# Optimization experiments

Hardware: AMD Instinct MI355X
Metric: run time of the kernel (lower is better)

The kernel has to match this reference:

```python
import jax, jax.numpy as jnp
import numpy as np


def conv1x1(x, w, b):
    # x: [B,C,H,W], w: [O,C], b: [O] -> [B,O,H,W]
    return jnp.einsum('bchw,oc->bohw', x, w) + b[None, :, None, None]


def setup_inputs() -> dict:
    key = jax.random.key(0)
    ks = jax.random.split(key, 8)
    B, C, H, W = 16, 256, 64, 64
    Cq = C // 8
    x = jax.random.normal(ks[0], (B, C, H, W), dtype=jnp.float32)
    wq = jax.random.normal(ks[1], (Cq, C), dtype=jnp.float32) * (2.0 / C) ** 0.5
    bq = jnp.zeros((Cq,), dtype=jnp.float32)
    wk = jax.random.normal(ks[2], (Cq, C), dtype=jnp.float32) * (2.0 / C) ** 0.5
    bk = jnp.zeros((Cq,), dtype=jnp.float32)
    wv = jax.random.normal(ks[3], (C, C), dtype=jnp.float32) * (2.0 / C) ** 0.5
    bv = jnp.zeros((C,), dtype=jnp.float32)
    gamma = jax.random.normal(ks[4], (1,), dtype=jnp.float32) * 0.1
    return {'x': x, 'wq': wq, 'bq': bq, 'wk': wk, 'bk': bk, 'wv': wv, 'bv': bv, 'gamma': gamma}


def reference(x, wq, bq, wk, bk, wv, bv, gamma):
    B, C, H, W = x.shape
    bH = B // 4
    bW = B // 4  # requires bH*bW == B, i.e. B == 16
    q = conv1x1(x, wq, bq)   # [B, C/8, H, W]
    k = conv1x1(x, wk, bk)   # [B, C/8, H, W]
    v = conv1x1(x, wv, bv)   # [B, C, H, W]
    # batch index b -> grid (h = b // bW, w = b % bW); token feature = flat map
    qg = q.reshape(bH, bW, -1)  # [bH, bW, Dq]
    kg = k.reshape(bH, bW, -1)
    vg = v.reshape(bH, bW, -1)  # [bH, bW, Dv]
    # column ('H') attention with -inf diagonal, row ('W') attention
    eH = jnp.einsum('hwd,gwd->hwg', qg, kg)  # [bH, bW, bH]
    eye = jnp.eye(bH, dtype=bool)[:, None, :]  # mask h == h'
    eH = jnp.where(eye, -jnp.inf, eH)
    eW = jnp.einsum('hwd,hgd->hwg', qg, kg)  # [bH, bW, bW]
    att = jax.nn.softmax(jnp.concatenate([eH, eW], axis=-1), axis=-1)
    aH, aW = att[..., :bH], att[..., bH:]
    oH = jnp.einsum('hwg,gwd->hwd', aH, vg)  # attend down the column
    oW = jnp.einsum('hwg,hgd->hwd', aW, vg)  # attend along the row
    out = (oH + oW).reshape(B, C, H, W)
    return gamma[0] * out + x
```

## Files before the change

### kernel.cpp

```cpp
#include <hip/hip_runtime.h>

#define HW_  4096
#define DQK  131072
#define DV   1048576

using bf16x8 = __attribute__((ext_vector_type(8))) __bf16;
using f32x4  = __attribute__((ext_vector_type(4))) float;
using u16x8  = __attribute__((ext_vector_type(8))) unsigned short;

static __device__ __forceinline__ unsigned short f2bf(float f) {
    union { float f; unsigned u; } v; v.f = f;
    unsigned r = v.u + 0x7FFFu + ((v.u >> 16) & 1u);
    return (unsigned short)(r >> 16);
}
static __device__ __forceinline__ float bf2f(unsigned short h) {
    union { unsigned u; float f; } v; v.u = ((unsigned)h) << 16;
    return v.f;
}

__global__ __launch_bounds__(256) void k_pack(const float* wq, const float* wk, const float* wv,
                                              unsigned short* WhF, unsigned short* WlF, unsigned short* WvF) {
    int idx = blockIdx.x * 256 + threadIdx.x;
    if (idx < 16384) {
        int i = idx;
        int mt = i >> 12, cg = (i >> 7) & 31, ml = (i >> 3) & 15, cl = i & 7;
        int m = mt * 16 + ml, c = cg * 8 + cl;
        float f = (m < 32) ? wq[m * 256 + c] : wk[(m - 32) * 256 + c];
        unsigned short hi = f2bf(f);
        WhF[i] = hi;
        WlF[i] = f2bf(f - bf2f(hi));
    } else {
        int i = idx - 16384;
        int mt = i >> 12, kt = (i >> 7) & 31, lr = (i >> 3) & 15, j = i & 7;
        int m = mt * 16 + lr, c = kt * 8 + j;
        WvF[i] = f2bf(wv[m * 256 + c]);
    }
}

__global__ __launch_bounds__(256) void k_gemm_qk(const unsigned short* __restrict__ WhF,
                                                 const unsigned short* __restrict__ WlF,
                                                 const float* __restrict__ x,
                                                 const float* __restrict__ bq, const float* __restrict__ bk,
                                                 float* __restrict__ QF, float* __restrict__ KF) {
    int b  = blockIdx.y;
    int n0 = blockIdx.x * 64;
    int t = threadIdx.x;
    int lane = t & 63, wid = t >> 6;
    int wm = wid & 1, wn = wid >> 1;
    int lr = lane & 15, kg = lane >> 4;

    const float* xb = x + (size_t)b * DV;
    const unsigned short* Ah0 = WhF + (size_t)(wm * 2) * 4096 + lane * 8;
    const unsigned short* Al0 = WlF + (size_t)(wm * 2) * 4096 + lane * 8;

    f32x4 acc[2][2];
    for (int mi = 0; mi < 2; mi++)
        for (int ni = 0; ni < 2; ni++) acc[mi][ni] = (f32x4){0.f, 0.f, 0.f, 0.f};

    for (int kk = 0; kk < 8; kk++) {
        bf16x8 ah[2], al[2];
        for (int mi = 0; mi < 2; mi++) {
            ah[mi] = *(const bf16x8*)(Ah0 + (size_t)mi * 4096 + kk * 512);
            al[mi] = *(const bf16x8*)(Al0 + (size_t)mi * 4096 + kk * 512);
        }
        bf16x8 bh[2], bl[2];
        int cbase = kk * 32 + kg * 8;
        for (int ni = 0; ni < 2; ni++) {
            const float* xp = xb + (size_t)cbase * HW_ + n0 + wn * 32 + ni * 16 + lr;
            #pragma unroll
            for (int j = 0; j < 8; j++) {
                float v = xp[(size_t)j * HW_];
                __bf16 h = (__bf16)v;
                bh[ni][j] = h;
                bl[ni][j] = (__bf16)(v - (float)h);
            }
        }
        for (int mi = 0; mi < 2; mi++)
            for (int ni = 0; ni < 2; ni++) {
                acc[mi][ni] = __builtin_amdgcn_mfma_f32_16x16x32_bf16(ah[mi], bh[ni], acc[mi][ni], 0, 0, 0);
                acc[mi][ni] = __builtin_amdgcn_mfma_f32_16x16x32_bf16(ah[mi], bl[ni], acc[mi][ni], 0, 0, 0);
                acc[mi][ni] = __builtin_amdgcn_mfma_f32_16x16x32_bf16(al[mi], bh[ni], acc[mi][ni], 0, 0, 0);
            }
    }

    float* dst = (wm == 0) ? QF : KF;
    const float* bias = (wm == 0) ? bq : bk;
    size_t base = (size_t)b * DQK + (size_t)blockIdx.x * 2048;
    for (int mi = 0; mi < 2; mi++) {
        f32x4 bvv = *(const f32x4*)(bias + mi * 16 + kg * 4);
        for (int ni = 0; ni < 2; ni++) {
            int slot = (wn * 2 + ni) * 2 + mi;
            f32x4 v = acc[mi][ni] + bvv;
            *(f32x4*)(dst + base + slot * 256 + lane * 4) = v;
        }
    }
}

__global__ __launch_bounds__(256) void k_scores2(const float* __restrict__ QF, const float* __restrict__ KF,
                                                 float* __restrict__ Sp) {
    __shared__ float Ql[16][520], Kl[16][520];
    int s = blockIdx.x;
    size_t off = (size_t)s * 512;
    int t = threadIdx.x;
    for (int b = 0; b < 16; b++) {
        const float* qs = QF + (size_t)b * DQK + off;
        const float* ks = KF + (size_t)b * DQK + off;
        Ql[b][t]       = qs[t];
        Ql[b][t + 256] = qs[t + 256];
        Kl[b][t]       = ks[t];
        Kl[b][t + 256] = ks[t + 256];
    }
    __syncthreads();
    int p = t >> 1, h = t & 1;
    int b = p >> 3, j = p & 7;
    int hb = b >> 2, wb = b & 3;
    int bp = (j < 4) ? (j * 4 + wb) : (hb * 4 + (j - 4));
    const f32x4* q4 = (const f32x4*)&Ql[b][h * 256];
    const f32x4* k4 = (const f32x4*)&Kl[bp][h * 256];
    f32x4 a4 = (f32x4){0.f, 0.f, 0.f, 0.f};
    for (int i = 0; i < 64; i++) a4 += q4[i] * k4[i];
    float sres = a4[0] + a4[1] + a4[2] + a4[3];
    sres += __shfl_xor(sres, 1);
    if (h == 0) Sp[(size_t)p * 256 + s] = sres;
}

__global__ void k_softmax2(const float* __restrict__ Sp, const float* __restrict__ gamma,
                           float* __restrict__ Mm) {
    __shared__ float SS[128];
    int t = threadIdx.x;
    const f32x4* s4 = (const f32x4*)(Sp + (size_t)t * 256);
    f32x4 a = (f32x4){0.f, 0.f, 0.f, 0.f};
    for (int i = 0; i < 64; i++) a += s4[i];
    SS[t] = a[0] + a[1] + a[2] + a[3];
    __syncthreads();
    if (t < 16) {
        int b = t, h = b >> 2, w = b & 3;
        float e[8];
        for (int j = 0; j < 8; j++) e[j] = SS[b * 8 + j];
        e[h] = -INFINITY;
        float mx = e[0];
        for (int j = 1; j < 8; j++) mx = fmaxf(mx, e[j]);
        float aa[8], sum = 0.f;
        for (int j = 0; j < 8; j++) { aa[j] = expf(e[j] - mx); sum += aa[j]; }
        float inv = 1.0f / sum;
        float g = gamma[0];
        float row[16];
        for (int c = 0; c < 16; c++) row[c] = 0.f;
        for (int gg = 0; gg < 4; gg++) if (gg != h) row[gg * 4 + w] += aa[gg] * inv;
        for (int gg = 0; gg < 4; gg++) row[h * 4 + gg] += aa[4 + gg] * inv;
        for (int c = 0; c < 16; c++) Mm[b * 16 + c] = row[c] * g;
        Mm[256 + b] = g;
    }
}

__global__ __launch_bounds__(256) void k_mix(const float* __restrict__ Mm, const float* __restrict__ x,
                                             unsigned short* __restrict__ Xm) {
    __shared__ float Ms[256];
    __shared__ __align__(16) unsigned short T[16][32][40];
    int t = threadIdx.x;
    int p0 = blockIdx.x * 32, c0 = blockIdx.y * 32;
    Ms[t] = Mm[t];

    int c_l = t >> 3, p4 = t & 7;
    f32x4 in4[16];
    for (int bp = 0; bp < 16; bp++)
        in4[bp] = *(const f32x4*)(x + (size_t)bp * DV + (size_t)(c0 + c_l) * HW_ + p0 + p4 * 4);
    __syncthreads();
    for (int b = 0; b < 16; b++) {
        int h = b >> 2, w = b & 3;
        f32x4 acc = (f32x4){0.f, 0.f, 0.f, 0.f};
        #pragma unroll
        for (int g = 0; g < 4; g++) {
            if (g != h) acc += Ms[b * 16 + g * 4 + w] * in4[g * 4 + w];
            acc += Ms[b * 16 + h * 4 + g] * in4[h * 4 + g];
        }
        for (int e = 0; e < 4; e++) T[b][p4 * 4 + e][c_l] = f2bf(acc[e]);
    }
    __syncthreads();
    int p_l = t & 31, co = (t >> 5) & 3, bh = t >> 7;
    int p = p0 + p_l;
    int c = c0 + co * 8;
    size_t dst = (size_t)(p >> 4) * 4096 + (size_t)(c >> 3) * 128 + (p & 15) * 8;
    #pragma unroll
    for (int bi = 0; bi < 8; bi++) {
        int b = bh * 8 + bi;
        u16x8 v = *(const u16x8*)&T[b][p_l][co * 8];
        *(u16x8*)(Xm + (size_t)b * DV + dst) = v;
    }
}

__global__ __launch_bounds__(512) void k_gemm_v_res(const unsigned short* __restrict__ WvF,
                                                    const unsigned short* __restrict__ XmF,
                                                    const float* __restrict__ bv,
                                                    const float* __restrict__ MmRs,
                                                    const float* __restrict__ x,
                                                    float* __restrict__ out) {
    __shared__ __align__(16) float LD[256][68];
    int b  = blockIdx.y;
    int n0 = blockIdx.x * 64;
    int t = threadIdx.x;
    int lane = t & 63, wid = t >> 6;
    int wm = wid >> 1, wn = wid & 1;
    int lr = lane & 15, kg = lane >> 4;

    const unsigned short* Bb = XmF + (size_t)b * DV + (size_t)(blockIdx.x * 4 + wn * 2) * 4096 + lane * 8;
    const unsigned short* Ab = WvF + (size_t)(wm * 4) * 4096 + lane * 8;

    bf16x8 bfr[8][2];
    #pragma unroll
    for (int kk = 0; kk < 8; kk++)
        #pragma unroll
        for (int ni = 0; ni < 2; ni++)
            bfr[kk][ni] = *(const bf16x8*)(Bb + (size_t)ni * 4096 + kk * 512);

    f32x4 acc[4][2];
    #pragma unroll
    for (int mi = 0; mi < 4; mi++)
        for (int ni = 0; ni < 2; ni++) acc[mi][ni] = (f32x4){0.f, 0.f, 0.f, 0.f};

    bf16x8 a[4], an[4];
    #pragma unroll
    for (int mi = 0; mi < 4; mi++) a[mi] = *(const bf16x8*)(Ab + (size_t)mi * 4096);
    #pragma unroll
    for (int kk = 0; kk < 8; kk++) {
        if (kk < 7) {
            #pragma unroll
            for (int mi = 0; mi < 4; mi++)
                an[mi] = *(const bf16x8*)(Ab + (size_t)mi * 4096 + (kk + 1) * 512);
        }
        #pragma unroll
        for (int mi = 0; mi < 4; mi++)
            #pragma unroll
            for (int ni = 0; ni < 2; ni++)
                acc[mi][ni] = __builtin_amdgcn_mfma_f32_16x16x32_bf16(a[mi], bfr[kk][ni], acc[mi][ni], 0, 0, 0);
        #pragma unroll
        for (int mi = 0; mi < 4; mi++) a[mi] = an[mi];
    }

    float rs = MmRs[256 + b];
    #pragma unroll
    for (int mi = 0; mi < 4; mi++) {
        int mrow0 = wm * 64 + mi * 16 + kg * 4;
        f32x4 bvv = *(const f32x4*)(bv + mrow0);
        #pragma unroll
        for (int ni = 0; ni < 2; ni++) {
            f32x4 mo = acc[mi][ni] + rs * bvv;
            int ncol = wn * 32 + ni * 16 + lr;
            #pragma unroll
            for (int i = 0; i < 4; i++) LD[mrow0 + i][ncol] = mo[i];
        }
    }
    __syncthreads();
    #pragma unroll
    for (int ps = 0; ps < 8; ps++) {
        int row = wid * 32 + ps * 4 + (lane >> 4);
        int nc  = (lane & 15) * 4;
        f32x4 o = *(const f32x4*)&LD[row][nc];
        size_t g = (size_t)b * DV + (size_t)row * HW_ + n0 + nc;
        f32x4 rr = *(const f32x4*)(x + g);
        __builtin_nontemporal_store(o + rr, (f32x4*)(out + g));
    }
}

extern "C" void kernel_launch(void* const* d_in, const int* in_sizes, int n_in,
                              void* d_out, int out_size, void* d_ws, size_t ws_size,
                              hipStream_t stream) {
    (void)in_sizes; (void)n_in; (void)out_size; (void)ws_size;
    const float* x     = (const float*)d_in[0];
    const float* wq    = (const float*)d_in[1];
    const float* bq    = (const float*)d_in[2];
    const float* wk    = (const float*)d_in[3];
    const float* bk    = (const float*)d_in[4];
    const float* wv    = (const float*)d_in[5];
    const float* bv    = (const float*)d_in[6];
    const float* gamma = (const float*)d_in[7];

    char* ws = (char*)d_ws;
    unsigned short* WhF = (unsigned short*)(ws + 0);
    unsigned short* WlF = (unsigned short*)(ws + 32768);
    unsigned short* WvF = (unsigned short*)(ws + 65536);
    float*          QF  = (float*)(ws + 196608);
    float*          KF  = (float*)(ws + 8585216);
    unsigned short* Xm  = (unsigned short*)(ws + 16973824);
    float*          Sp  = (float*)(ws + 16973824);
    float*          Mm  = (float*)(ws + 0);
    float*          vo  = (float*)d_out;

    k_pack       <<<320, 256, 0, stream>>>(wq, wk, wv, WhF, WlF, WvF);
    k_gemm_qk    <<<dim3(64, 16), 256, 0, stream>>>(WhF, WlF, x, bq, bk, QF, KF);
    k_scores2    <<<256, 256, 0, stream>>>(QF, KF, Sp);
    k_softmax2   <<<1, 128, 0, stream>>>(Sp, gamma, Mm);
    k_mix        <<<dim3(128, 8), 256, 0, stream>>>(Mm, x, Xm);
    k_gemm_v_res <<<dim3(64, 16), 512, 0, stream>>>(WvF, Xm, bv, Mm, x, vo);
}
```

Measured before the change: 85.95 us.

## Fuse weight packing and softmax into neighboring kernels to cut launches

Removes the separate weight-pack and softmax kernels. The Q/K GEMM now reads fp32 weights directly and splits them into hi/lo bf16 in registers. The softmax runs in the last block of the scores kernel, chosen through an atomic ticket. Packing of the V weight moves into extra blocks of the mix kernel. Dropping two launches (one of them a single-block serial kernel) should cut launch and serialization overhead, at the cost of redundant weight conversion per GEMM block and an atomic plus fences in the scores kernel.

```diff
diff --git a/kernel.cpp b/kernel.cpp
--- a/kernel.cpp
+++ b/kernel.cpp
@@ -13,35 +13,14 @@
     unsigned r = v.u + 0x7FFFu + ((v.u >> 16) & 1u);
     return (unsigned short)(r >> 16);
 }
-static __device__ __forceinline__ float bf2f(unsigned short h) {
-    union { unsigned u; float f; } v; v.u = ((unsigned)h) << 16;
-    return v.f;
-}
-
-__global__ __launch_bounds__(256) void k_pack(const float* wq, const float* wk, const float* wv,
-                                              unsigned short* WhF, unsigned short* WlF, unsigned short* WvF) {
-    int idx = blockIdx.x * 256 + threadIdx.x;
-    if (idx < 16384) {
-        int i = idx;
-        int mt = i >> 12, cg = (i >> 7) & 31, ml = (i >> 3) & 15, cl = i & 7;
-        int m = mt * 16 + ml, c = cg * 8 + cl;
-        float f = (m < 32) ? wq[m * 256 + c] : wk[(m - 32) * 256 + c];
-        unsigned short hi = f2bf(f);
-        WhF[i] = hi;
-        WlF[i] = f2bf(f - bf2f(hi));
-    } else {
-        int i = idx - 16384;
-        int mt = i >> 12, kt = (i >> 7) & 31, lr = (i >> 3) & 15, j = i & 7;
-        int m = mt * 16 + lr, c = kt * 8 + j;
-        WvF[i] = f2bf(wv[m * 256 + c]);
-    }
-}
-
-__global__ __launch_bounds__(256) void k_gemm_qk(const unsigned short* __restrict__ WhF,
-                                                 const unsigned short* __restrict__ WlF,
+
+__global__ __launch_bounds__(256) void k_gemm_qk(const float* __restrict__ wq,
+                                                 const float* __restrict__ wk,
                                                  const float* __restrict__ x,
                                                  const float* __restrict__ bq, const float* __restrict__ bk,
-                                                 float* __restrict__ QF, float* __restrict__ KF) {
+                                                 float* __restrict__ QF, float* __restrict__ KF,
+                                                 unsigned int* __restrict__ ticket) {
+    if (blockIdx.x == 0 && blockIdx.y == 0 && threadIdx.x == 0) *ticket = 0u;
     int b  = blockIdx.y;
     int n0 = blockIdx.x * 64;
     int t = threadIdx.x;
@@ -50,8 +29,7 @@
     int lr = lane & 15, kg = lane >> 4;
 
     const float* xb = x + (size_t)b * DV;
-    const unsigned short* Ah0 = WhF + (size_t)(wm * 2) * 4096 + lane * 8;
-    const unsigned short* Al0 = WlF + (size_t)(wm * 2) * 4096 + lane * 8;
+    const float* wsrc = (wm == 0) ? wq : wk;
 
     f32x4 acc[2][2];
     for (int mi = 0; mi < 2; mi++)
@@ -60,8 +38,18 @@
     for (int kk = 0; kk < 8; kk++) {
         bf16x8 ah[2], al[2];
         for (int mi = 0; mi < 2; mi++) {
-            ah[mi] = *(const bf16x8*)(Ah0 + (size_t)mi * 4096 + kk * 512);
-            al[mi] = *(const bf16x8*)(Al0 + (size_t)mi * 4096 + kk * 512);
+            const float* wp = wsrc + (size_t)(mi * 16 + lr) * 256 + kk * 32 + kg * 8;
+            f32x4 w0 = *(const f32x4*)(wp);
+            f32x4 w1 = *(const f32x4*)(wp + 4);
+            #pragma unroll
+            for (int j = 0; j < 4; j++) {
+                __bf16 h0 = (__bf16)w0[j];
+                ah[mi][j] = h0;
+                al[mi][j] = (__bf16)(w0[j] - (float)h0);
+                __bf16 h1 = (__bf16)w1[j];
+                ah[mi][j + 4] = h1;
+                al[mi][j + 4] = (__bf16)(w1[j] - (float)h1);
+            }
         }
         bf16x8 bh[2], bl[2];
         int cbase = kk * 32 + kg * 8;
@@ -96,9 +84,12 @@
     }
 }
 
-__global__ __launch_bounds__(256) void k_scores2(const float* __restrict__ QF, const float* __restrict__ KF,
-                                                 float* __restrict__ Sp) {
+__global__ __launch_bounds__(256) void k_scores3(const float* __restrict__ QF, const float* __restrict__ KF,
+                                                 const float* __restrict__ gamma,
+                                                 float* __restrict__ Sp, float* __restrict__ Mm,
+                                                 unsigned int* __restrict__ ticket) {
     __shared__ float Ql[16][520], Kl[16][520];
+    __shared__ unsigned int isLast;
     int s = blockIdx.x;
     size_t off = (size_t)s * 512;
     int t = threadIdx.x;
@@ -111,54 +102,71 @@
         Kl[b][t + 256] = ks[t + 256];
     }
     __syncthreads();
-    int p = t >> 1, h = t & 1;
-    int b = p >> 3, j = p & 7;
-    int hb = b >> 2, wb = b & 3;
-    int bp = (j < 4) ? (j * 4 + wb) : (hb * 4 + (j - 4));
-    const f32x4* q4 = (const f32x4*)&Ql[b][h * 256];
-    const f32x4* k4 = (const f32x4*)&Kl[bp][h * 256];
-    f32x4 a4 = (f32x4){0.f, 0.f, 0.f, 0.f};
-    for (int i = 0; i < 64; i++) a4 += q4[i] * k4[i];
-    float sres = a4[0] + a4[1] + a4[2] + a4[3];
-    sres += __shfl_xor(sres, 1);
-    if (h == 0) Sp[(size_t)p * 256 + s] = sres;
-}
-
-__global__ void k_softmax2(const float* __restrict__ Sp, const float* __restrict__ gamma,
-                           float* __restrict__ Mm) {
-    __shared__ float SS[128];
+    {
+        int p = t >> 1, h = t & 1;
+        int b = p >> 3, j = p & 7;
+        int hb = b >> 2, wb = b & 3;
+        int bp = (j < 4) ? (j * 4 + wb) : (hb * 4 + (j - 4));
+        const f32x4* q4 = (const f32x4*)&Ql[b][h * 256];
+        const f32x4* k4 = (const f32x4*)&Kl[bp][h * 256];
+        f32x4 a4 = (f32x4){0.f, 0.f, 0.f, 0.f};
+        for (int i = 0; i < 64; i++) a4 += q4[i] * k4[i];
+        float sres = a4[0] + a4[1] + a4[2] + a4[3];
+        sres += __shfl_xor(sres, 1);
+        if (h == 0) Sp[(size_t)p * 256 + s] = sres;
+    }
+    __threadfence();
+    if (t == 0) isLast = (atomicAdd(ticket, 1u) == 255u) ? 1u : 0u;
+    __syncthreads();
+    if (isLast) {
+        __threadfence();
+        __shared__ float SS[128];
+        if (t < 128) {
+            const f32x4* s4 = (const f32x4*)(Sp + (size_t)t * 256);
+            f32x4 a = (f32x4){0.f, 0.f, 0.f, 0.f};
+            for (int i = 0; i < 64; i++) a += s4[i];
+            SS[t] = a[0] + a[1] + a[2] + a[3];
+        }
+        __syncthreads();
+        if (t < 16) {
+            int b = t, h = b >> 2, w = b & 3;
+            float e[8];
+            for (int j = 0; j < 8; j++) e[j] = SS[b * 8 + j];
+            e[h] = -INFINITY;
+            float mx = e[0];
+            for (int j = 1; j < 8; j++) mx = fmaxf(mx, e[j]);
+            float aa[8], sum = 0.f;
+            for (int j = 0; j < 8; j++) { aa[j] = expf(e[j] - mx); sum += aa[j]; }
+            float inv = 1.0f / sum;
+            float g = gamma[0];
+            float row[16];
+            for (int c = 0; c < 16; c++) row[c] = 0.f;
+            for (int gg = 0; gg < 4; gg++) if (gg != h) row[gg * 4 + w] += aa[gg] * inv;
+            for (int gg = 0; gg < 4; gg++) row[h * 4 + gg] += aa[4 + gg] * inv;
+            for (int c = 0; c < 16; c++) Mm[b * 16 + c] = row[c] * g;
+            Mm[256 + b] = g;
+        }
+    }
+}
+
+__global__ __launch_bounds__(256) void k_mix(const float* __restrict__ Mm, const float* __restrict__ x,
+                                             const float* __restrict__ wv,
+                                             unsigned short* __restrict__ Xm,
+                                             unsigned short* __restrict__ WvF) {
+    int bid = blockIdx.x;
     int t = threadIdx.x;
-    const f32x4* s4 = (const f32x4*)(Sp + (size_t)t * 256);
-    f32x4 a = (f32x4){0.f, 0.f, 0.f, 0.f};
-    for (int i = 0; i < 64; i++) a += s4[i];
-    SS[t] = a[0] + a[1] + a[2] + a[3];
-    __syncthreads();
-    if (t < 16) {
-        int b = t, h = b >> 2, w = b & 3;
-        float e[8];
-        for (int j = 0; j < 8; j++) e[j] = SS[b * 8 + j];
-        e[h] = -INFINITY;
-        float mx = e[0];
-        for (int j = 1; j < 8; j++) mx = fmaxf(mx, e[j]);
-        float aa[8], sum = 0.f;
-        for (int j = 0; j < 8; j++) { aa[j] = expf(e[j] - mx); sum += aa[j]; }
-        float inv = 1.0f / sum;
-        float g = gamma[0];
-        float row[16];
-        for (int c = 0; c < 16; c++) row[c] = 0.f;
-        for (int gg = 0; gg < 4; gg++) if (gg != h) row[gg * 4 + w] += aa[gg] * inv;
-        for (int gg = 0; gg < 4; gg++) row[h * 4 + gg] += aa[4 + gg] * inv;
-        for (int c = 0; c < 16; c++) Mm[b * 16 + c] = row[c] * g;
-        Mm[256 + b] = g;
-    }
-}
-
-__global__ __launch_bounds__(256) void k_mix(const float* __restrict__ Mm, const float* __restrict__ x,
-                                             unsigned short* __restrict__ Xm) {
+    if (bid >= 1024) {
+        int chunk = (bid - 1024) * 16384;
+        for (int i = t; i < 16384; i += 256) {
+            int ii = chunk + i;
+            int mt = ii >> 12, kt = (ii >> 7) & 31, lr = (ii >> 3) & 15, j = ii & 7;
+            WvF[ii] = f2bf(wv[(mt * 16 + lr) * 256 + kt * 8 + j]);
+        }
+        return;
+    }
     __shared__ float Ms[256];
     __shared__ __align__(16) unsigned short T[16][32][40];
-    int t = threadIdx.x;
-    int p0 = blockIdx.x * 32, c0 = blockIdx.y * 32;
+    int p0 = (bid & 127) * 32, c0 = (bid >> 7) * 32;
     Ms[t] = Mm[t];
 
     int c_l = t >> 3, p4 = t & 7;
@@ -276,20 +284,17 @@
     const float* gamma = (const float*)d_in[7];
 
     char* ws = (char*)d_ws;
-    unsigned short* WhF = (unsigned short*)(ws + 0);
-    unsigned short* WlF = (unsigned short*)(ws + 32768);
-    unsigned short* WvF = (unsigned short*)(ws + 65536);
-    float*          QF  = (float*)(ws + 196608);
-    float*          KF  = (float*)(ws + 8585216);
-    unsigned short* Xm  = (unsigned short*)(ws + 16973824);
-    float*          Sp  = (float*)(ws + 16973824);
-    float*          Mm  = (float*)(ws + 0);
-    float*          vo  = (float*)d_out;
-
-    k_pack       <<<320, 256, 0, stream>>>(wq, wk, wv, WhF, WlF, WvF);
-    k_gemm_qk    <<<dim3(64, 16), 256, 0, stream>>>(WhF, WlF, x, bq, bk, QF, KF);
-    k_scores2    <<<256, 256, 0, stream>>>(QF, KF, Sp);
-    k_softmax2   <<<1, 128, 0, stream>>>(Sp, gamma, Mm);
-    k_mix        <<<dim3(128, 8), 256, 0, stream>>>(Mm, x, Xm);
+    unsigned short* WvF    = (unsigned short*)(ws + 0);
+    float*          QF     = (float*)(ws + 131072);
+    float*          KF     = (float*)(ws + 8519680);
+    float*          Mm     = (float*)(ws + 16908288);
+    unsigned int*   ticket = (unsigned int*)(ws + 16909376);
+    unsigned short* Xm     = (unsigned short*)(ws + 16910336);
+    float*          Sp     = (float*)(ws + 16910336);
+    float*          vo     = (float*)d_out;
+
+    k_gemm_qk    <<<dim3(64, 16), 256, 0, stream>>>(wq, wk, x, bq, bk, QF, KF, ticket);
+    k_scores3    <<<256, 256, 0, stream>>>(QF, KF, gamma, Sp, Mm, ticket);
+    k_mix        <<<1032, 256, 0, stream>>>(Mm, x, wv, Xm, WvF);
     k_gemm_v_res <<<dim3(64, 16), 512, 0, stream>>>(WvF, Xm, bv, Mm, x, vo);
 }
```

Result: slower. 120.9 us (+40.7%).

## Stage x tile through swizzled LDS with vectorized loads and register prefetch

Applied to the files above, without the earlier changes.

The QK projection GEMM previously had every wave load x with scalar strided global reads and convert each element to hi/lo bf16 itself, so the two waves sharing an N slice both reloaded the same data. Now each thread issues float4 loads of x, splits them into hi/lo bf16 once, and writes them to XOR-swizzled shared memory tiles. The waves then read bf16x8 fragments from LDS, and the next k-slice is prefetched into registers while the MFMAs run. In exchange this adds two barriers per k-step, some LDS footprint and a launch-bounds occupancy hint.

```diff
diff --git a/kernel.cpp b/kernel.cpp
--- a/kernel.cpp
+++ b/kernel.cpp
@@ -37,11 +37,12 @@
     }
 }
 
-__global__ __launch_bounds__(256) void k_gemm_qk(const unsigned short* __restrict__ WhF,
-                                                 const unsigned short* __restrict__ WlF,
-                                                 const float* __restrict__ x,
-                                                 const float* __restrict__ bq, const float* __restrict__ bk,
-                                                 float* __restrict__ QF, float* __restrict__ KF) {
+__global__ __launch_bounds__(256, 4) void k_gemm_qk(const unsigned short* __restrict__ WhF,
+                                                    const unsigned short* __restrict__ WlF,
+                                                    const float* __restrict__ x,
+                                                    const float* __restrict__ bq, const float* __restrict__ bk,
+                                                    float* __restrict__ QF, float* __restrict__ KF) {
+    __shared__ __align__(16) __bf16 Bh[64][40], Bl[64][40];
     int b  = blockIdx.y;
     int n0 = blockIdx.x * 64;
     int t = threadIdx.x;
@@ -49,45 +50,72 @@
     int wm = wid & 1, wn = wid >> 1;
     int lr = lane & 15, kg = lane >> 4;
 
-    const float* xb = x + (size_t)b * DV;
+    int nl = t & 15, cr = t >> 4;
+    const float* xs = x + (size_t)b * DV + n0 + nl * 4;
+
     const unsigned short* Ah0 = WhF + (size_t)(wm * 2) * 4096 + lane * 8;
     const unsigned short* Al0 = WlF + (size_t)(wm * 2) * 4096 + lane * 8;
 
     f32x4 acc[2][2];
+    #pragma unroll
     for (int mi = 0; mi < 2; mi++)
+        #pragma unroll
         for (int ni = 0; ni < 2; ni++) acc[mi][ni] = (f32x4){0.f, 0.f, 0.f, 0.f};
 
+    f32x4 v0 = *(const f32x4*)(xs + (size_t)cr * HW_);
+    f32x4 v1 = *(const f32x4*)(xs + (size_t)(16 + cr) * HW_);
+
+    int oct0 = cr >> 3, oct1 = (16 + cr) >> 3, cb = cr & 7, nl3 = nl & 3;
+
+    #pragma unroll
     for (int kk = 0; kk < 8; kk++) {
+        #pragma unroll
+        for (int e = 0; e < 4; e++) {
+            int n  = nl * 4 + e;
+            int s0 = (oct0 ^ e ^ nl3) * 8 + cb;
+            int s1 = (oct1 ^ e ^ nl3) * 8 + cb;
+            float f0 = v0[e]; __bf16 h0 = (__bf16)f0;
+            Bh[n][s0] = h0; Bl[n][s0] = (__bf16)(f0 - (float)h0);
+            float f1 = v1[e]; __bf16 h1 = (__bf16)f1;
+            Bh[n][s1] = h1; Bl[n][s1] = (__bf16)(f1 - (float)h1);
+        }
+        __syncthreads();
+        if (kk < 7) {
+            v0 = *(const f32x4*)(xs + (size_t)((kk + 1) * 32 + cr) * HW_);
+            v1 = *(const f32x4*)(xs + (size_t)((kk + 1) * 32 + 16 + cr) * HW_);
+        }
         bf16x8 ah[2], al[2];
+        #pragma unroll
         for (int mi = 0; mi < 2; mi++) {
             ah[mi] = *(const bf16x8*)(Ah0 + (size_t)mi * 4096 + kk * 512);
             al[mi] = *(const bf16x8*)(Al0 + (size_t)mi * 4096 + kk * 512);
         }
         bf16x8 bh[2], bl[2];
-        int cbase = kk * 32 + kg * 8;
+        #pragma unroll
         for (int ni = 0; ni < 2; ni++) {
-            const float* xp = xb + (size_t)cbase * HW_ + n0 + wn * 32 + ni * 16 + lr;
+            int n  = wn * 32 + ni * 16 + lr;
+            int co = (kg ^ (n & 3) ^ ((n >> 2) & 3)) * 8;
+            bh[ni] = *(const bf16x8*)&Bh[n][co];
+            bl[ni] = *(const bf16x8*)&Bl[n][co];
+        }
+        #pragma unroll
+        for (int mi = 0; mi < 2; mi++)
             #pragma unroll
-            for (int j = 0; j < 8; j++) {
-                float v = xp[(size_t)j * HW_];
-                __bf16 h = (__bf16)v;
-                bh[ni][j] = h;
-                bl[ni][j] = (__bf16)(v - (float)h);
-            }
-        }
-        for (int mi = 0; mi < 2; mi++)
             for (int ni = 0; ni < 2; ni++) {
                 acc[mi][ni] = __builtin_amdgcn_mfma_f32_16x16x32_bf16(ah[mi], bh[ni], acc[mi][ni], 0, 0, 0);
                 acc[mi][ni] = __builtin_amdgcn_mfma_f32_16x16x32_bf16(ah[mi], bl[ni], acc[mi][ni], 0, 0, 0);
                 acc[mi][ni] = __builtin_amdgcn_mfma_f32_16x16x32_bf16(al[mi], bh[ni], acc[mi][ni], 0, 0, 0);
             }
+        __syncthreads();
     }
 
     float* dst = (wm == 0) ? QF : KF;
     const float* bias = (wm == 0) ? bq : bk;
     size_t base = (size_t)b * DQK + (size_t)blockIdx.x * 2048;
+    #pragma unroll
     for (int mi = 0; mi < 2; mi++) {
         f32x4 bvv = *(const f32x4*)(bias + mi * 16 + kg * 4);
+        #pragma unroll
         for (int ni = 0; ni < 2; ni++) {
             int slot = (wn * 2 + ni) * 2 + mi;
             f32x4 v = acc[mi][ni] + bvv;
```

New measurement: 86.54 us. About the same (+0.7%).
